# Optimization experiments

Measured on AMD Instinct MI355X. Metric: run time of the kernel, lower is better.

The kernel has to match this reference:

```python
import jax, jax.numpy as jnp
import numpy as np

HIDDEN = 2048
HEADS = 16
HEAD_DIM = HIDDEN // HEADS
BATCH = 2
SEQ = 2048


def setup_inputs() -> dict:
    key = jax.random.key(0)
    ks = jax.random.split(key, 9)
    s = 0.02
    return {
        "x": jax.random.normal(ks[0], (BATCH, SEQ, HIDDEN), dtype=jnp.float32),
        "Wq": jax.random.normal(ks[1], (HIDDEN, HIDDEN), dtype=jnp.float32) * s,
        "bq": jax.random.normal(ks[2], (HIDDEN,), dtype=jnp.float32) * s,
        "Wk": jax.random.normal(ks[3], (HIDDEN, HIDDEN), dtype=jnp.float32) * s,
        "bk": jax.random.normal(ks[4], (HIDDEN,), dtype=jnp.float32) * s,
        "Wv": jax.random.normal(ks[5], (HIDDEN, HIDDEN), dtype=jnp.float32) * s,
        "bv": jax.random.normal(ks[6], (HIDDEN,), dtype=jnp.float32) * s,
        "Wo": jax.random.normal(ks[7], (HIDDEN, HIDDEN), dtype=jnp.float32) * s,
        "bo": jax.random.normal(ks[8], (HIDDEN,), dtype=jnp.float32) * s,
    }


def reference(x, Wq, bq, Wk, bk, Wv, bv, Wo, bo):
    B, S, H = x.shape
    # Linear layers: y = x @ W.T + b (torch nn.Linear convention, W:[out,in])
    q = x @ Wq.T + bq
    k = x @ Wk.T + bk
    v = x @ Wv.T + bv
    # [B, S, H] -> [B, nH, S, hd]
    def split_heads(t):
        return t.reshape(B, S, HEADS, HEAD_DIM).transpose(0, 2, 1, 3)
    q, k, v = split_heads(q), split_heads(k), split_heads(v)
    scale = 1.0 / (HEAD_DIM ** 0.5)
    # NOTE: original module applies NO causal mask despite its name; be faithful.
    scores = jnp.einsum('bhqd,bhkd->bhqk', q, k) * scale
    probs = jax.nn.softmax(scores, axis=-1)
    attn = jnp.einsum('bhqk,bhkd->bhqd', probs, v)
    attn = attn.transpose(0, 2, 1, 3).reshape(B, S, H)
    return attn @ Wo.T + bo
```

## Files before the change

kernel.cpp:

```cpp
#include <hip/hip_runtime.h>
#include <hip/hip_bf16.h>
#include <stdint.h>

typedef __bf16 bf16_t;
typedef __attribute__((ext_vector_type(8))) __bf16 bf16x8;
typedef __attribute__((ext_vector_type(4))) float floatx4;
typedef __attribute__((ext_vector_type(16))) float f32x16;
typedef __attribute__((ext_vector_type(2))) int i32x2;

typedef __attribute__((address_space(1))) const unsigned int gu32_t;
typedef __attribute__((address_space(3))) unsigned int lu32_t;

__device__ __forceinline__ void async16(const void* g, void* l) {
    __builtin_amdgcn_global_load_lds((gu32_t*)g, (lu32_t*)l, 16, 0, 0);
}

__device__ __forceinline__ uint32_t pack2(float lo, float hi) {
    union { bf16_t h[2]; uint32_t u; } cv;
    cv.h[0] = (bf16_t)lo; cv.h[1] = (bf16_t)hi;
    return cv.u;
}

__global__ __launch_bounds__(256) void cvt_f32_bf16(const float* __restrict__ in,
                                                    bf16_t* __restrict__ out) {
    int i = (blockIdx.x * 256 + threadIdx.x) * 8;
    float4 a = *(const float4*)(in + i);
    float4 b = *(const float4*)(in + i + 4);
    bf16x8 v;
    v[0] = (bf16_t)a.x; v[1] = (bf16_t)a.y; v[2] = (bf16_t)a.z; v[3] = (bf16_t)a.w;
    v[4] = (bf16_t)b.x; v[5] = (bf16_t)b.y; v[6] = (bf16_t)b.z; v[7] = (bf16_t)b.w;
    *(bf16x8*)(out + i) = v;
}

__global__ __launch_bounds__(256) void cvt4_f32_bf16(const float* __restrict__ w0,
                                                     const float* __restrict__ w1,
                                                     const float* __restrict__ w2,
                                                     const float* __restrict__ w3,
                                                     bf16_t* __restrict__ out,
                                                     int elems) {
    const float* srcs[4] = {w0, w1, w2, w3};
    const float* in = srcs[blockIdx.y];
    bf16_t* o = out + (size_t)blockIdx.y * elems;
    int i = (blockIdx.x * 256 + threadIdx.x) * 8;
    float4 a = *(const float4*)(in + i);
    float4 b = *(const float4*)(in + i + 4);
    bf16x8 v;
    v[0] = (bf16_t)a.x; v[1] = (bf16_t)a.y; v[2] = (bf16_t)a.z; v[3] = (bf16_t)a.w;
    v[4] = (bf16_t)b.x; v[5] = (bf16_t)b.y; v[6] = (bf16_t)b.z; v[7] = (bf16_t)b.w;
    *(bf16x8*)(o + i) = v;
}

template <bool OUT_F32, bool BIAS_ROW>
__global__ __launch_bounds__(256) void gemm_bt(const bf16_t* __restrict__ A,
                                               const bf16_t* __restrict__ B,
                                               const float* __restrict__ bias,
                                               const float* __restrict__ bias2,
                                               int nsplit, float scaleA, float scaleB,
                                               float* __restrict__ Cf,
                                               bf16_t* __restrict__ Cb,
                                               int M, int N, int K, int ldc) {
    __shared__ bf16_t As[128 * 64];
    __shared__ bf16_t Bs[128 * 64];
    const int tid = threadIdx.x;
    const int wave = tid >> 6, lane = tid & 63;
    const int quad = lane >> 4, l16 = lane & 15;
    const int wm = (wave >> 1) * 64, wn = (wave & 1) * 64;
    const int tm = blockIdx.x * 128, tn = blockIdx.y * 128;

    floatx4 acc[4][4];
#pragma unroll
    for (int i = 0; i < 4; ++i)
#pragma unroll
        for (int j = 0; j < 4; ++j) acc[i][j] = floatx4{0.f, 0.f, 0.f, 0.f};

    const bf16_t* Abase = A + (size_t)tm * K;
    const bf16_t* Bbase = B + (size_t)tn * K;
    const int sw = l16 & 7;

    for (int kk = 0; kk < K; kk += 64) {
#pragma unroll
        for (int it = 0; it < 4; ++it) {
            int chunk = it * 256 + tid;
            int r = chunk >> 3, c = chunk & 7;
            int c2 = c ^ (r & 7);
            async16(Abase + r * K + kk + c2 * 8, As + (it * 256 + wave * 64) * 8);
            async16(Bbase + r * K + kk + c2 * 8, Bs + (it * 256 + wave * 64) * 8);
        }
        __syncthreads();
#pragma unroll
        for (int ks = 0; ks < 2; ++ks) {
            bf16x8 af[4], bf[4];
#pragma unroll
            for (int mt = 0; mt < 4; ++mt)
                af[mt] = *(const bf16x8*)(As + (wm + mt * 16 + l16) * 64 +
                                          ((ks * 4 + quad) ^ sw) * 8);
#pragma unroll
            for (int nt = 0; nt < 4; ++nt)
                bf[nt] = *(const bf16x8*)(Bs + (wn + nt * 16 + l16) * 64 +
                                          ((ks * 4 + quad) ^ sw) * 8);
#pragma unroll
            for (int mt = 0; mt < 4; ++mt)
#pragma unroll
                for (int nt = 0; nt < 4; ++nt)
                    acc[mt][nt] = __builtin_amdgcn_mfma_f32_16x16x32_bf16(af[mt], bf[nt],
                                                                          acc[mt][nt], 0, 0, 0);
        }
        __syncthreads();
    }
#pragma unroll
    for (int mt = 0; mt < 4; ++mt)
#pragma unroll
        for (int nt = 0; nt < 4; ++nt)
#pragma unroll
            for (int r = 0; r < 4; ++r) {
                int row = tm + wm + mt * 16 + quad * 4 + r;
                int col = tn + wn + nt * 16 + l16;
                float bv = BIAS_ROW ? bias[row]
                                    : (col < nsplit ? bias[col] : bias2[col - nsplit]);
                float v = acc[mt][nt][r] + bv;
                if (!BIAS_ROW) v *= (col < nsplit ? scaleA : scaleB);
                if (OUT_F32) Cf[(size_t)row * ldc + col] = v;
                else Cb[(size_t)row * ldc + col] = (bf16_t)v;
            }
}

template <bool OUT_F32>
__global__ __launch_bounds__(512, 2) void gemm256(const bf16_t* __restrict__ A,
                                                  const bf16_t* __restrict__ B,
                                                  const float* __restrict__ bias,
                                                  const float* __restrict__ bias2,
                                                  int nsplit, float scaleA, float scaleB,
                                                  float* __restrict__ Cf,
                                                  bf16_t* __restrict__ Cb,
                                                  int M, int N, int K, int ldc) {
    __shared__ bf16_t As[2][256 * 64];
    __shared__ bf16_t Bs[2][256 * 64];
    const int tid = threadIdx.x;
    const int wave = tid >> 6, lane = tid & 63;
    const int quad = lane >> 4, l16 = lane & 15;
    const int wr = wave >> 2, wc = wave & 3;
    const int nbx = M >> 8, nby = N >> 8;
    const int nwg = nbx * nby;
    const int xcd = blockIdx.x & 7, idx = blockIdx.x >> 3;
    const int per = nwg >> 3;
    const int wg = xcd * per + idx;
    const int tm = (wg % nbx) * 256, tn = (wg / nbx) * 256;

    floatx4 acc[8][4];
#pragma unroll
    for (int i = 0; i < 8; ++i)
#pragma unroll
        for (int j = 0; j < 4; ++j) acc[i][j] = floatx4{0.f, 0.f, 0.f, 0.f};

    const bf16_t* Abase = A + (size_t)tm * K;
    const bf16_t* Bbase = B + (size_t)tn * K;
    const int sw = l16 & 7;
    const int NT = K >> 6;

    auto stageA = [&](int kk, int b) {
#pragma unroll
        for (int it = 0; it < 4; ++it) {
            int chunk = it * 512 + tid;
            int r = chunk >> 3, c = chunk & 7;
            int c2 = c ^ (r & 7);
            async16(Abase + (size_t)r * K + kk + c2 * 8, As[b] + chunk * 8);
        }
    };
    auto stageB = [&](int kk, int b) {
#pragma unroll
        for (int it = 0; it < 4; ++it) {
            int chunk = it * 512 + tid;
            int r = chunk >> 3, c = chunk & 7;
            int c2 = c ^ (r & 7);
            async16(Bbase + (size_t)r * K + kk + c2 * 8, Bs[b] + chunk * 8);
        }
    };

    stageA(0, 0);
    stageB(0, 0);
    asm volatile("s_waitcnt vmcnt(0)" ::: "memory");
    __builtin_amdgcn_s_barrier();
    __builtin_amdgcn_sched_barrier(0);

    for (int t = 0; t < NT; ++t) {
        const int cur = t & 1;
        const bf16_t* Asb = As[cur];
        const bf16_t* Bsb = Bs[cur];
        const int nk = (t + 1) << 6;
        const bool more = (t + 1 < NT);
#pragma unroll
        for (int p = 0; p < 4; ++p) {
            const int mh = p >> 1, nh = p & 1;
            bf16x8 af[4][2], bf[2][2];
#pragma unroll
            for (int mt = 0; mt < 4; ++mt) {
                int row = wr * 128 + mh * 64 + mt * 16 + l16;
#pragma unroll
                for (int ks = 0; ks < 2; ++ks)
                    af[mt][ks] = *(const bf16x8*)(Asb + row * 64 + ((ks * 4 + quad) ^ sw) * 8);
            }
#pragma unroll
            for (int nt = 0; nt < 2; ++nt) {
                int col = wc * 64 + nh * 32 + nt * 16 + l16;
#pragma unroll
                for (int ks = 0; ks < 2; ++ks)
                    bf[nt][ks] = *(const bf16x8*)(Bsb + col * 64 + ((ks * 4 + quad) ^ sw) * 8);
            }
            if (more) {
                if (p == 0) stageA(nk, cur ^ 1);
                else if (p == 1) stageB(nk, cur ^ 1);
            }
            __builtin_amdgcn_s_barrier();
            asm volatile("s_waitcnt lgkmcnt(0)" ::: "memory");
            __builtin_amdgcn_sched_barrier(0);
            __builtin_amdgcn_s_setprio(1);
#pragma unroll
            for (int ks = 0; ks < 2; ++ks)
#pragma unroll
                for (int mt = 0; mt < 4; ++mt)
#pragma unroll
                    for (int nt = 0; nt < 2; ++nt)
                        acc[mh * 4 + mt][nh * 2 + nt] =
                            __builtin_amdgcn_mfma_f32_16x16x32_bf16(
                                af[mt][ks], bf[nt][ks], acc[mh * 4 + mt][nh * 2 + nt], 0, 0, 0);
            __builtin_amdgcn_s_setprio(0);
            if (p == 3 && more)
                asm volatile("s_waitcnt vmcnt(0)" ::: "memory");
            __builtin_amdgcn_s_barrier();
            __builtin_amdgcn_sched_barrier(0);
        }
    }

#pragma unroll
    for (int am = 0; am < 8; ++am)
#pragma unroll
        for (int an = 0; an < 4; ++an)
#pragma unroll
            for (int r = 0; r < 4; ++r) {
                int row = tm + wr * 128 + (am >> 2) * 64 + (am & 3) * 16 + quad * 4 + r;
                int col = tn + wc * 64 + (an >> 1) * 32 + (an & 1) * 16 + l16;
                float bv = col < nsplit ? bias[col] : bias2[col - nsplit];
                float v = (acc[am][an][r] + bv) * (col < nsplit ? scaleA : scaleB);
                if (OUT_F32) Cf[(size_t)row * ldc + col] = v;
                else Cb[(size_t)row * ldc + col] = (bf16_t)v;
            }
}

#define KELEMS (64 * 128)
#define VELEMS (128 * 64)
__global__ __launch_bounds__(256, 2) void flash_attn(const bf16_t* __restrict__ Qp,
                                                     const bf16_t* __restrict__ Kp,
                                                     const bf16_t* __restrict__ Vt,
                                                     bf16_t* __restrict__ O) {
    __shared__ bf16_t smem[2 * KELEMS + 2 * VELEMS];
    const int tid = threadIdx.x;
    const int wv = tid >> 6, lane = tid & 63;
    const int hi = lane >> 5, l32 = lane & 31;
    const int wq = wv >> 1, wk = wv & 1;
    const int LD = 4096, T = 4096, S = 2048, HO = 2048;

    const int gid = blockIdx.x;
    const int kq = gid >> 3;
    const int qt = kq & 31;
    const int grp = (gid & 7) + 8 * (kq >> 5);
    const int hd = grp & 15, bt = grp >> 4;

    const int qrow0 = bt * S + qt * 64;
    const int krow0 = bt * S;
    const int hoff = hd * 128;
    const int sw7 = l32 & 7;
    const int swK = l32 & 15;

    bf16x8 qf[8];
    const bf16_t* qptr = Qp + (size_t)(qrow0 + wq * 32 + l32) * LD + hoff + hi * 8;
#pragma unroll
    for (int ks = 0; ks < 8; ++ks) qf[ks] = *(const bf16x8*)(qptr + ks * 16);

    float l_i = 0.f;
    f32x16 Oacc[4];
#pragma unroll
    for (int dt = 0; dt < 4; ++dt)
#pragma unroll
        for (int r = 0; r < 16; ++r) Oacc[dt][r] = 0.f;

    auto stageK = [&](int kt, int b) {
        int kb = krow0 + kt * 64;
        bf16_t* Ks = smem + b * KELEMS;
#pragma unroll
        for (int it = 0; it < 4; ++it) {
            int chunk = it * 256 + tid;
            int r = chunk >> 4, c = chunk & 15;
            int c2 = c ^ (r & 15);
            async16(Kp + (size_t)(kb + r) * LD + hoff + c2 * 8, Ks + chunk * 8);
        }
    };
    auto stageV = [&](int kt, int b) {
        int kb = krow0 + kt * 64;
        bf16_t* Vts = smem + 2 * KELEMS + b * VELEMS;
#pragma unroll
        for (int it = 0; it < 4; ++it) {
            int chunk = it * 256 + tid;
            int r = chunk >> 3, c = chunk & 7;
            int c2 = c ^ (r & 7);
            async16(Vt + (size_t)(hoff + r) * T + kb + c2 * 8, Vts + chunk * 8);
        }
    };

    auto pv = [&](const uint32_t* pk, int vb) {
        const bf16_t* Vts = smem + 2 * KELEMS + vb * VELEMS;
        __builtin_amdgcn_s_setprio(1);
#pragma unroll
        for (int s = 0; s < 2; ++s) {
            i32x2 s02 = __builtin_amdgcn_permlane32_swap((int)pk[4 * s + 0],
                                                         (int)pk[4 * s + 2], false, false);
            i32x2 s13 = __builtin_amdgcn_permlane32_swap((int)pk[4 * s + 1],
                                                         (int)pk[4 * s + 3], false, false);
            union { uint32_t u[4]; bf16x8 v; } w;
            w.u[0] = (uint32_t)s02[0];
            w.u[1] = (uint32_t)s13[0];
            w.u[2] = (uint32_t)s02[1];
            w.u[3] = (uint32_t)s13[1];
#pragma unroll
            for (int dt = 0; dt < 4; ++dt) {
                bf16x8 a = *(const bf16x8*)(Vts + (dt * 32 + l32) * 64 +
                                            ((4 * wk + 2 * s + hi) ^ sw7) * 8);
                Oacc[dt] = __builtin_amdgcn_mfma_f32_32x32x16_bf16(a, w.v, Oacc[dt], 0, 0, 0);
            }
        }
        __builtin_amdgcn_s_setprio(0);
    };

    uint32_t pkPrev[8];
    stageK(0, 0);
    stageV(0, 0);
    for (int kt = 0; kt < 32; ++kt) {
        const int cur = kt & 1;
        __syncthreads();
        if (kt + 1 < 32) stageK(kt + 1, cur ^ 1);

        const bf16_t* Ks = smem + cur * KELEMS;

        f32x16 sf0, sf1;
#pragma unroll
        for (int r = 0; r < 16; ++r) { sf0[r] = 0.f; sf1[r] = 0.f; }
        __builtin_amdgcn_s_setprio(1);
#pragma unroll
        for (int ks = 0; ks < 4; ++ks) {
            bf16x8 a0 = *(const bf16x8*)(Ks + (wk * 32 + l32) * 128 +
                                         ((2 * ks + hi) ^ swK) * 8);
            bf16x8 a1 = *(const bf16x8*)(Ks + (wk * 32 + l32) * 128 +
                                         ((2 * (ks + 4) + hi) ^ swK) * 8);
            sf0 = __builtin_amdgcn_mfma_f32_32x32x16_bf16(a0, qf[ks], sf0, 0, 0, 0);
            sf1 = __builtin_amdgcn_mfma_f32_32x32x16_bf16(a1, qf[ks + 4], sf1, 0, 0, 0);
        }
        __builtin_amdgcn_s_setprio(0);

        if (kt > 0) pv(pkPrev, cur ^ 1);

        __syncthreads();
        if (kt + 1 < 32) stageV(kt + 1, cur ^ 1);

        float rs0 = 0.f, rs1 = 0.f;
#pragma unroll
        for (int a4 = 0; a4 < 4; ++a4) {
            float p0 = exp2f(sf0[4 * a4 + 0] + sf1[4 * a4 + 0]);
            float p1 = exp2f(sf0[4 * a4 + 1] + sf1[4 * a4 + 1]);
            float p2 = exp2f(sf0[4 * a4 + 2] + sf1[4 * a4 + 2]);
            float p3 = exp2f(sf0[4 * a4 + 3] + sf1[4 * a4 + 3]);
            rs0 += p0 + p1;
            rs1 += p2 + p3;
            pkPrev[a4 * 2 + 0] = pack2(p0, p1);
            pkPrev[a4 * 2 + 1] = pack2(p2, p3);
        }
        l_i += rs0 + rs1;
    }

    pv(pkPrev, 1);

    __syncthreads();
    l_i += __shfl_xor(l_i, 32);
    float* ml = (float*)smem;
    if (hi == 0) ml[wv * 32 + l32] = l_i;
    __syncthreads();
    float linv = 1.0f / (l_i + ml[(wv ^ 1) * 32 + l32]);
    __syncthreads();

    float* Op = (float*)smem;
    if (wk == 1) {
#pragma unroll
        for (int dt = 0; dt < 4; ++dt)
#pragma unroll
            for (int r = 0; r < 16; ++r) {
                int d = dt * 32 + (r & 3) + 8 * (r >> 2) + 4 * hi;
                Op[(wq * 128 + d) * 32 + l32] = Oacc[dt][r];
            }
    }
    __syncthreads();
    if (wk == 0) {
#pragma unroll
        for (int dt = 0; dt < 4; ++dt)
#pragma unroll
            for (int r = 0; r < 16; ++r) {
                int d = dt * 32 + (r & 3) + 8 * (r >> 2) + 4 * hi;
                Oacc[dt][r] = (Oacc[dt][r] + Op[(wq * 128 + d) * 32 + l32]) * linv;
            }
    }
    __syncthreads();

    if (wk == 0) {
        uint32_t* Os = (uint32_t*)smem + wq * 2048;
#pragma unroll
        for (int dt = 0; dt < 4; ++dt)
#pragma unroll
            for (int a4 = 0; a4 < 4; ++a4) {
                uint32_t q0 = pack2(Oacc[dt][4 * a4 + 0], Oacc[dt][4 * a4 + 1]);
                uint32_t q1 = pack2(Oacc[dt][4 * a4 + 2], Oacc[dt][4 * a4 + 3]);
                int d2 = 16 * dt + 4 * a4 + 2 * hi;
                Os[l32 * 64 + ((d2 + 2 * l32) & 63)] = q0;
                Os[l32 * 64 + ((d2 + 1 + 2 * l32) & 63)] = q1;
            }
#pragma unroll
        for (int r = 0; r < 32; ++r) {
            uint32_t v = Os[r * 64 + ((lane + 2 * r) & 63)];
            uint32_t* orow = (uint32_t*)(O + (size_t)(qrow0 + wq * 32 + r) * HO + hoff);
            orow[lane] = v;
        }
    }
}

extern "C" void kernel_launch(void* const* d_in, const int* in_sizes, int n_in,
                              void* d_out, int out_size, void* d_ws, size_t ws_size,
                              hipStream_t stream) {
    const float* x  = (const float*)d_in[0];
    const float* Wq = (const float*)d_in[1];
    const float* bq = (const float*)d_in[2];
    const float* Wk = (const float*)d_in[3];
    const float* bk = (const float*)d_in[4];
    const float* Wv = (const float*)d_in[5];
    const float* bv = (const float*)d_in[6];
    const float* Wo = (const float*)d_in[7];
    const float* bo = (const float*)d_in[8];
    float* out = (float*)d_out;

    const int T = 4096;
    const int H = 2048;
    const float SL2E = 0.088388347688f * 1.44269504089f;
    bf16_t* ws  = (bf16_t*)d_ws;
    bf16_t* xb  = ws;
    bf16_t* wqb = xb  + (size_t)T * H;
    bf16_t* wkb = wqb + (size_t)H * H;
    bf16_t* wvb = wkb + (size_t)H * H;
    bf16_t* wob = wvb + (size_t)H * H;
    bf16_t* QKb = wob + (size_t)H * H;
    bf16_t* Vtb = QKb + (size_t)T * 2 * H;
    bf16_t* Ab  = Vtb + (size_t)H * T;
    size_t need = (size_t)(Ab + (size_t)T * H - ws) * sizeof(bf16_t);
    if (ws_size < need) return;

    cvt_f32_bf16<<<T * H / 2048, 256, 0, stream>>>(x, xb);
    cvt4_f32_bf16<<<dim3(H * H / 2048, 4), 256, 0, stream>>>(Wq, Wk, Wv, Wo, wqb, H * H);

    gemm256<false><<<(T / 256) * (4096 / 256), 512, 0, stream>>>(
        xb, wqb, bq, bk, H, SL2E, 1.0f, nullptr, QKb, T, 4096, H, 4096);

    dim3 gv(H / 128, T / 128);
    gemm_bt<false, true><<<gv, 256, 0, stream>>>(wvb, xb, bv, nullptr, 0, 1.0f, 1.0f,
                                                 nullptr, Vtb, H, T, H, T);

    flash_attn<<<1024, 256, 0, stream>>>(QKb, QKb + H, Vtb, Ab);

    dim3 go(T / 128, H / 128);
    gemm_bt<true, false><<<go, 256, 0, stream>>>(Ab, wob, bo, nullptr, H, 1.0f, 1.0f,
                                                 out, nullptr, T, H, H, H);
}
```

Measured before the change: 399.7 us.

## Generalize pipelined 8-wave GEMM for V and O projections; triple-buffer V in attention

Replaces the simple single-buffered 128x128 GEMM used for the V projection and output projection with a templated 512-thread, double-buffered GEMM with XCD-aware tile mapping, using 128x256 and 256x128 tiles. The flash attention kernel gets a third V buffer so K and V for the next tile are staged together after one barrier, which removes the second per-iteration __syncthreads. Priority hints are also removed. The costs are more LDS per attention block, which may lower occupancy, and more complex buffer-index bookkeeping.

```diff
diff --git a/kernel.cpp b/kernel.cpp
--- a/kernel.cpp
+++ b/kernel.cpp
@@ -50,105 +50,35 @@
     *(bf16x8*)(o + i) = v;
 }
 
-template <bool OUT_F32, bool BIAS_ROW>
-__global__ __launch_bounds__(256) void gemm_bt(const bf16_t* __restrict__ A,
-                                               const bf16_t* __restrict__ B,
-                                               const float* __restrict__ bias,
-                                               const float* __restrict__ bias2,
-                                               int nsplit, float scaleA, float scaleB,
-                                               float* __restrict__ Cf,
-                                               bf16_t* __restrict__ Cb,
-                                               int M, int N, int K, int ldc) {
-    __shared__ bf16_t As[128 * 64];
-    __shared__ bf16_t Bs[128 * 64];
+template <bool OUT_F32, bool BIAS_ROW, int BM, int BN>
+__global__ __launch_bounds__(512, 2) void gemm8p(const bf16_t* __restrict__ A,
+                                                 const bf16_t* __restrict__ B,
+                                                 const float* __restrict__ bias,
+                                                 const float* __restrict__ bias2,
+                                                 int nsplit, float scaleA, float scaleB,
+                                                 float* __restrict__ Cf,
+                                                 bf16_t* __restrict__ Cb,
+                                                 int M, int N, int K, int ldc) {
+    constexpr int WC = BN / 64;
+    constexpr int WR = 8 / WC;
+    constexpr int WAVE_M = BM / WR;
+    constexpr int MT = WAVE_M / 16;
+    __shared__ bf16_t As[2][BM * 64];
+    __shared__ bf16_t Bs[2][BN * 64];
     const int tid = threadIdx.x;
     const int wave = tid >> 6, lane = tid & 63;
     const int quad = lane >> 4, l16 = lane & 15;
-    const int wm = (wave >> 1) * 64, wn = (wave & 1) * 64;
-    const int tm = blockIdx.x * 128, tn = blockIdx.y * 128;
-
-    floatx4 acc[4][4];
-#pragma unroll
-    for (int i = 0; i < 4; ++i)
-#pragma unroll
-        for (int j = 0; j < 4; ++j) acc[i][j] = floatx4{0.f, 0.f, 0.f, 0.f};
-
-    const bf16_t* Abase = A + (size_t)tm * K;
-    const bf16_t* Bbase = B + (size_t)tn * K;
-    const int sw = l16 & 7;
-
-    for (int kk = 0; kk < K; kk += 64) {
-#pragma unroll
-        for (int it = 0; it < 4; ++it) {
-            int chunk = it * 256 + tid;
-            int r = chunk >> 3, c = chunk & 7;
-            int c2 = c ^ (r & 7);
-            async16(Abase + r * K + kk + c2 * 8, As + (it * 256 + wave * 64) * 8);
-            async16(Bbase + r * K + kk + c2 * 8, Bs + (it * 256 + wave * 64) * 8);
-        }
-        __syncthreads();
-#pragma unroll
-        for (int ks = 0; ks < 2; ++ks) {
-            bf16x8 af[4], bf[4];
-#pragma unroll
-            for (int mt = 0; mt < 4; ++mt)
-                af[mt] = *(const bf16x8*)(As + (wm + mt * 16 + l16) * 64 +
-                                          ((ks * 4 + quad) ^ sw) * 8);
-#pragma unroll
-            for (int nt = 0; nt < 4; ++nt)
-                bf[nt] = *(const bf16x8*)(Bs + (wn + nt * 16 + l16) * 64 +
-                                          ((ks * 4 + quad) ^ sw) * 8);
-#pragma unroll
-            for (int mt = 0; mt < 4; ++mt)
-#pragma unroll
-                for (int nt = 0; nt < 4; ++nt)
-                    acc[mt][nt] = __builtin_amdgcn_mfma_f32_16x16x32_bf16(af[mt], bf[nt],
-                                                                          acc[mt][nt], 0, 0, 0);
-        }
-        __syncthreads();
-    }
-#pragma unroll
-    for (int mt = 0; mt < 4; ++mt)
-#pragma unroll
-        for (int nt = 0; nt < 4; ++nt)
-#pragma unroll
-            for (int r = 0; r < 4; ++r) {
-                int row = tm + wm + mt * 16 + quad * 4 + r;
-                int col = tn + wn + nt * 16 + l16;
-                float bv = BIAS_ROW ? bias[row]
-                                    : (col < nsplit ? bias[col] : bias2[col - nsplit]);
-                float v = acc[mt][nt][r] + bv;
-                if (!BIAS_ROW) v *= (col < nsplit ? scaleA : scaleB);
-                if (OUT_F32) Cf[(size_t)row * ldc + col] = v;
-                else Cb[(size_t)row * ldc + col] = (bf16_t)v;
-            }
-}
-
-template <bool OUT_F32>
-__global__ __launch_bounds__(512, 2) void gemm256(const bf16_t* __restrict__ A,
-                                                  const bf16_t* __restrict__ B,
-                                                  const float* __restrict__ bias,
-                                                  const float* __restrict__ bias2,
-                                                  int nsplit, float scaleA, float scaleB,
-                                                  float* __restrict__ Cf,
-                                                  bf16_t* __restrict__ Cb,
-                                                  int M, int N, int K, int ldc) {
-    __shared__ bf16_t As[2][256 * 64];
-    __shared__ bf16_t Bs[2][256 * 64];
-    const int tid = threadIdx.x;
-    const int wave = tid >> 6, lane = tid & 63;
-    const int quad = lane >> 4, l16 = lane & 15;
-    const int wr = wave >> 2, wc = wave & 3;
-    const int nbx = M >> 8, nby = N >> 8;
-    const int nwg = nbx * nby;
+    const int wr = wave / WC, wc = wave % WC;
+    const int nbx = M / BM;
+    const int nwg = nbx * (N / BN);
     const int xcd = blockIdx.x & 7, idx = blockIdx.x >> 3;
     const int per = nwg >> 3;
     const int wg = xcd * per + idx;
-    const int tm = (wg % nbx) * 256, tn = (wg / nbx) * 256;
-
-    floatx4 acc[8][4];
-#pragma unroll
-    for (int i = 0; i < 8; ++i)
+    const int tm = (wg % nbx) * BM, tn = (wg / nbx) * BN;
+
+    floatx4 acc[MT][4];
+#pragma unroll
+    for (int i = 0; i < MT; ++i)
 #pragma unroll
         for (int j = 0; j < 4; ++j) acc[i][j] = floatx4{0.f, 0.f, 0.f, 0.f};
 
@@ -158,8 +88,9 @@
     const int NT = K >> 6;
 
     auto stageA = [&](int kk, int b) {
-#pragma unroll
-        for (int it = 0; it < 4; ++it) {
+        constexpr int IT = BM / 64;
+#pragma unroll
+        for (int it = 0; it < IT; ++it) {
             int chunk = it * 512 + tid;
             int r = chunk >> 3, c = chunk & 7;
             int c2 = c ^ (r & 7);
@@ -167,8 +98,9 @@
         }
     };
     auto stageB = [&](int kk, int b) {
-#pragma unroll
-        for (int it = 0; it < 4; ++it) {
+        constexpr int IT = BN / 64;
+#pragma unroll
+        for (int it = 0; it < IT; ++it) {
             int chunk = it * 512 + tid;
             int r = chunk >> 3, c = chunk & 7;
             int c2 = c ^ (r & 7);
@@ -188,59 +120,100 @@
         const bf16_t* Bsb = Bs[cur];
         const int nk = (t + 1) << 6;
         const bool more = (t + 1 < NT);
-#pragma unroll
-        for (int p = 0; p < 4; ++p) {
-            const int mh = p >> 1, nh = p & 1;
-            bf16x8 af[4][2], bf[2][2];
-#pragma unroll
-            for (int mt = 0; mt < 4; ++mt) {
-                int row = wr * 128 + mh * 64 + mt * 16 + l16;
+        if constexpr (MT == 8) {
+#pragma unroll
+            for (int p = 0; p < 4; ++p) {
+                const int mh = p >> 1, nh = p & 1;
+                bf16x8 af[4][2], bg[2][2];
+#pragma unroll
+                for (int mt = 0; mt < 4; ++mt) {
+                    int row = wr * 128 + mh * 64 + mt * 16 + l16;
+#pragma unroll
+                    for (int ks = 0; ks < 2; ++ks)
+                        af[mt][ks] = *(const bf16x8*)(Asb + row * 64 + ((ks * 4 + quad) ^ sw) * 8);
+                }
+#pragma unroll
+                for (int nt = 0; nt < 2; ++nt) {
+                    int col = wc * 64 + nh * 32 + nt * 16 + l16;
+#pragma unroll
+                    for (int ks = 0; ks < 2; ++ks)
+                        bg[nt][ks] = *(const bf16x8*)(Bsb + col * 64 + ((ks * 4 + quad) ^ sw) * 8);
+                }
+                if (more) {
+                    if (p == 0) stageA(nk, cur ^ 1);
+                    else if (p == 1) stageB(nk, cur ^ 1);
+                }
+                __builtin_amdgcn_s_barrier();
+                asm volatile("s_waitcnt lgkmcnt(0)" ::: "memory");
+                __builtin_amdgcn_sched_barrier(0);
+                __builtin_amdgcn_s_setprio(1);
 #pragma unroll
                 for (int ks = 0; ks < 2; ++ks)
-                    af[mt][ks] = *(const bf16x8*)(Asb + row * 64 + ((ks * 4 + quad) ^ sw) * 8);
-            }
-#pragma unroll
-            for (int nt = 0; nt < 2; ++nt) {
-                int col = wc * 64 + nh * 32 + nt * 16 + l16;
-#pragma unroll
-                for (int ks = 0; ks < 2; ++ks)
-                    bf[nt][ks] = *(const bf16x8*)(Bsb + col * 64 + ((ks * 4 + quad) ^ sw) * 8);
-            }
-            if (more) {
-                if (p == 0) stageA(nk, cur ^ 1);
-                else if (p == 1) stageB(nk, cur ^ 1);
-            }
-            __builtin_amdgcn_s_barrier();
-            asm volatile("s_waitcnt lgkmcnt(0)" ::: "memory");
-            __builtin_amdgcn_sched_barrier(0);
-            __builtin_amdgcn_s_setprio(1);
-#pragma unroll
-            for (int ks = 0; ks < 2; ++ks)
+#pragma unroll
+                    for (int mt = 0; mt < 4; ++mt)
+#pragma unroll
+                        for (int nt = 0; nt < 2; ++nt)
+                            acc[mh * 4 + mt][nh * 2 + nt] =
+                                __builtin_amdgcn_mfma_f32_16x16x32_bf16(
+                                    af[mt][ks], bg[nt][ks], acc[mh * 4 + mt][nh * 2 + nt], 0, 0, 0);
+                __builtin_amdgcn_s_setprio(0);
+                if (p == 3 && more)
+                    asm volatile("s_waitcnt vmcnt(0)" ::: "memory");
+                __builtin_amdgcn_s_barrier();
+                __builtin_amdgcn_sched_barrier(0);
+            }
+        } else {
+#pragma unroll
+            for (int p = 0; p < 2; ++p) {
+                bf16x8 af[4], bg[4];
+#pragma unroll
+                for (int mt = 0; mt < 4; ++mt) {
+                    int row = wr * 64 + mt * 16 + l16;
+                    af[mt] = *(const bf16x8*)(Asb + row * 64 + ((p * 4 + quad) ^ sw) * 8);
+                }
+#pragma unroll
+                for (int nt = 0; nt < 4; ++nt) {
+                    int col = wc * 64 + nt * 16 + l16;
+                    bg[nt] = *(const bf16x8*)(Bsb + col * 64 + ((p * 4 + quad) ^ sw) * 8);
+                }
+                if (more && p == 0) { stageA(nk, cur ^ 1); stageB(nk, cur ^ 1); }
+                __builtin_amdgcn_s_barrier();
+                asm volatile("s_waitcnt lgkmcnt(0)" ::: "memory");
+                __builtin_amdgcn_sched_barrier(0);
+                __builtin_amdgcn_s_setprio(1);
 #pragma unroll
                 for (int mt = 0; mt < 4; ++mt)
 #pragma unroll
-                    for (int nt = 0; nt < 2; ++nt)
-                        acc[mh * 4 + mt][nh * 2 + nt] =
-                            __builtin_amdgcn_mfma_f32_16x16x32_bf16(
-                                af[mt][ks], bf[nt][ks], acc[mh * 4 + mt][nh * 2 + nt], 0, 0, 0);
-            __builtin_amdgcn_s_setprio(0);
-            if (p == 3 && more)
-                asm volatile("s_waitcnt vmcnt(0)" ::: "memory");
-            __builtin_amdgcn_s_barrier();
-            __builtin_amdgcn_sched_barrier(0);
+                    for (int nt = 0; nt < 4; ++nt)
+                        acc[mt][nt] = __builtin_amdgcn_mfma_f32_16x16x32_bf16(
+                            af[mt], bg[nt], acc[mt][nt], 0, 0, 0);
+                __builtin_amdgcn_s_setprio(0);
+                if (p == 1 && more)
+                    asm volatile("s_waitcnt vmcnt(0)" ::: "memory");
+                __builtin_amdgcn_s_barrier();
+                __builtin_amdgcn_sched_barrier(0);
+            }
         }
     }
 
 #pragma unroll
-    for (int am = 0; am < 8; ++am)
+    for (int am = 0; am < MT; ++am)
 #pragma unroll
         for (int an = 0; an < 4; ++an)
 #pragma unroll
             for (int r = 0; r < 4; ++r) {
-                int row = tm + wr * 128 + (am >> 2) * 64 + (am & 3) * 16 + quad * 4 + r;
-                int col = tn + wc * 64 + (an >> 1) * 32 + (an & 1) * 16 + l16;
-                float bv = col < nsplit ? bias[col] : bias2[col - nsplit];
-                float v = (acc[am][an][r] + bv) * (col < nsplit ? scaleA : scaleB);
+                int row, col;
+                if constexpr (MT == 8) {
+                    row = tm + wr * 128 + (am >> 2) * 64 + (am & 3) * 16 + quad * 4 + r;
+                    col = tn + wc * 64 + (an >> 1) * 32 + (an & 1) * 16 + l16;
+                } else {
+                    row = tm + wr * 64 + am * 16 + quad * 4 + r;
+                    col = tn + wc * 64 + an * 16 + l16;
+                }
+                float bv = BIAS_ROW ? bias[row]
+                                    : (col < nsplit ? bias[col] : bias2[col - nsplit]);
+                float v = acc[am][an][r] + bv;
+                if (!BIAS_ROW) v *= (col < nsplit ? scaleA : scaleB);
                 if (OUT_F32) Cf[(size_t)row * ldc + col] = v;
                 else Cb[(size_t)row * ldc + col] = (bf16_t)v;
             }
@@ -252,7 +225,7 @@
                                                      const bf16_t* __restrict__ Kp,
                                                      const bf16_t* __restrict__ Vt,
                                                      bf16_t* __restrict__ O) {
-    __shared__ bf16_t smem[2 * KELEMS + 2 * VELEMS];
+    __shared__ bf16_t smem[2 * KELEMS + 3 * VELEMS];
     const int tid = threadIdx.x;
     const int wv = tid >> 6, lane = tid & 63;
     const int hi = lane >> 5, l32 = lane & 31;
@@ -308,7 +281,6 @@
 
     auto pv = [&](const uint32_t* pk, int vb) {
         const bf16_t* Vts = smem + 2 * KELEMS + vb * VELEMS;
-        __builtin_amdgcn_s_setprio(1);
 #pragma unroll
         for (int s = 0; s < 2; ++s) {
             i32x2 s02 = __builtin_amdgcn_permlane32_swap((int)pk[4 * s + 0],
@@ -327,23 +299,26 @@
                 Oacc[dt] = __builtin_amdgcn_mfma_f32_32x32x16_bf16(a, w.v, Oacc[dt], 0, 0, 0);
             }
         }
-        __builtin_amdgcn_s_setprio(0);
     };
 
     uint32_t pkPrev[8];
+    int vcur = 0;
     stageK(0, 0);
     stageV(0, 0);
     for (int kt = 0; kt < 32; ++kt) {
-        const int cur = kt & 1;
+        const int kcur = kt & 1;
         __syncthreads();
-        if (kt + 1 < 32) stageK(kt + 1, cur ^ 1);
-
-        const bf16_t* Ks = smem + cur * KELEMS;
+        if (kt + 1 < 32) {
+            int vnxt = (vcur == 2) ? 0 : vcur + 1;
+            stageK(kt + 1, kcur ^ 1);
+            stageV(kt + 1, vnxt);
+        }
+
+        const bf16_t* Ks = smem + kcur * KELEMS;
 
         f32x16 sf0, sf1;
 #pragma unroll
         for (int r = 0; r < 16; ++r) { sf0[r] = 0.f; sf1[r] = 0.f; }
-        __builtin_amdgcn_s_setprio(1);
 #pragma unroll
         for (int ks = 0; ks < 4; ++ks) {
             bf16x8 a0 = *(const bf16x8*)(Ks + (wk * 32 + l32) * 128 +
@@ -353,12 +328,8 @@
             sf0 = __builtin_amdgcn_mfma_f32_32x32x16_bf16(a0, qf[ks], sf0, 0, 0, 0);
             sf1 = __builtin_amdgcn_mfma_f32_32x32x16_bf16(a1, qf[ks + 4], sf1, 0, 0, 0);
         }
-        __builtin_amdgcn_s_setprio(0);
-
-        if (kt > 0) pv(pkPrev, cur ^ 1);
-
-        __syncthreads();
-        if (kt + 1 < 32) stageV(kt + 1, cur ^ 1);
+
+        if (kt > 0) pv(pkPrev, (vcur == 0) ? 2 : vcur - 1);
 
         float rs0 = 0.f, rs1 = 0.f;
 #pragma unroll
@@ -373,9 +344,11 @@
             pkPrev[a4 * 2 + 1] = pack2(p2, p3);
         }
         l_i += rs0 + rs1;
+
+        if (kt + 1 < 32) vcur = (vcur == 2) ? 0 : vcur + 1;
     }
 
-    pv(pkPrev, 1);
+    pv(pkPrev, vcur);
 
     __syncthreads();
     l_i += __shfl_xor(l_i, 32);
@@ -460,16 +433,14 @@
     cvt_f32_bf16<<<T * H / 2048, 256, 0, stream>>>(x, xb);
     cvt4_f32_bf16<<<dim3(H * H / 2048, 4), 256, 0, stream>>>(Wq, Wk, Wv, Wo, wqb, H * H);
 
-    gemm256<false><<<(T / 256) * (4096 / 256), 512, 0, stream>>>(
+    gemm8p<false, false, 256, 256><<<(T / 256) * (4096 / 256), 512, 0, stream>>>(
         xb, wqb, bq, bk, H, SL2E, 1.0f, nullptr, QKb, T, 4096, H, 4096);
 
-    dim3 gv(H / 128, T / 128);
-    gemm_bt<false, true><<<gv, 256, 0, stream>>>(wvb, xb, bv, nullptr, 0, 1.0f, 1.0f,
-                                                 nullptr, Vtb, H, T, H, T);
+    gemm8p<false, true, 128, 256><<<(H / 128) * (T / 256), 512, 0, stream>>>(
+        wvb, xb, bv, nullptr, 0, 1.0f, 1.0f, nullptr, Vtb, H, T, H, T);
 
     flash_attn<<<1024, 256, 0, stream>>>(QKb, QKb + H, Vtb, Ab);
 
-    dim3 go(T / 128, H / 128);
-    gemm_bt<true, false><<<go, 256, 0, stream>>>(Ab, wob, bo, nullptr, H, 1.0f, 1.0f,
-                                                 out, nullptr, T, H, H, H);
-}
+    gemm8p<true, false, 256, 128><<<(T / 256) * (H / 128), 512, 0, stream>>>(
+        Ab, wob, bo, nullptr, H, 1.0f, 1.0f, out, nullptr, T, H, H, H);
+}
```

After: 409.3 us. +2.4%, slower.
